# Kernel optimization log

Measured on AMD Instinct MI355X. Metric: run time of the kernel, lower is better.

## Reference

```python
import jax, jax.numpy as jnp
import numpy as np

EPS = 0.05
N = 33554432  # 2**25 annotation steps


def setup_inputs() -> dict:
    key = jax.random.key(0)
    # categories in 1..5 (cat==0 is a no-op skip in the original loop; excluding it
    # keeps the output length static at N+1)
    annotation_series = jax.random.randint(key, (N,), 1, 6, dtype=jnp.int64 if jax.config.jax_enable_x64 else jnp.int32)
    # learned scalar weights of the six Linear(1,1,bias=False) layers, at their init constants
    return {
        "annotation_series": annotation_series,
        "origin_w": jnp.asarray(0.0, jnp.float32),
        "big_decrease_w": jnp.asarray(-0.3, jnp.float32),
        "decrease_w": jnp.asarray(-0.1, jnp.float32),
        "same_w": jnp.asarray(0.0, jnp.float32),
        "increase_w": jnp.asarray(0.1, jnp.float32),
        "big_increase_w": jnp.asarray(0.3, jnp.float32),
    }


def _change_table(origin_w, bd, d, s, inc, bi):
    sg = jax.lax.stop_gradient  # clamp bounds came from .item() in torch -> detached
    c1 = jnp.minimum(bd, sg(jnp.minimum(0.0, d))) - EPS                 # big decrease
    c2 = jnp.clip(d, sg(bd) + EPS, 0.0 - EPS)                           # decrease
    c3 = s                                                              # same
    c4 = jnp.clip(inc, 0.0 + EPS, sg(bi) - EPS)                         # increase
    c5 = jnp.maximum(bi, sg(jnp.maximum(0.0, inc)) + EPS)               # big increase
    zero = jnp.zeros_like(c1)  # cat 0 unused (inputs restricted to 1..5)
    return jnp.stack([zero, c1, c2, c3, c4, c5])  # [6]


def reference(annotation_series, origin_w, big_decrease_w, decrease_w, same_w, increase_w, big_increase_w):
    table = _change_table(origin_w, big_decrease_w, decrease_w, same_w, increase_w, big_increase_w)
    changes = table[annotation_series]                    # [N] gather from 6-entry LUT
    series = origin_w + jnp.cumsum(changes)               # [N] inclusive prefix sum
    return jnp.concatenate([origin_w[None], series])      # [N+1]
```

## Files before the change

kernel.cpp:

```cpp
#include <hip/hip_runtime.h>

#define EPS_C 0.05f
#define BLOCK 256
#define SUBT 2
#define CHUNK (SUBT * 4096)

__device__ __forceinline__ void build_table(const float* bd_p, const float* d_p,
                                            const float* s_p, const float* inc_p,
                                            const float* bi_p, float* cs) {
  if (threadIdx.x == 0) {
    float bd = *bd_p, d = *d_p, s = *s_p, inc = *inc_p, bi = *bi_p;
    cs[0] = 0.0f;
    cs[1] = fminf(bd, fminf(0.0f, d)) - EPS_C;
    cs[2] = fminf(fmaxf(d, bd + EPS_C), -EPS_C);
    cs[3] = s;
    cs[4] = fminf(fmaxf(inc, EPS_C), bi - EPS_C);
    cs[5] = fmaxf(bi, fmaxf(0.0f, inc) + EPS_C);
    cs[6] = 0.0f; cs[7] = 0.0f;
  }
}

__global__ __launch_bounds__(BLOCK) void k_reduce_pack(
    const int* __restrict__ ann, const float* bd, const float* d,
    const float* s, const float* inc, const float* bi,
    uint2* __restrict__ packed, float* __restrict__ sums) {
  __shared__ float cs[8];
  __shared__ float wsum[BLOCK / 64];
  build_table(bd, d, s, inc, bi, cs);
  __syncthreads();

  const int b = blockIdx.x, t = threadIdx.x;
  const int4* in4 = (const int4*)(ann + (size_t)b * CHUNK);

  float sum = 0.0f;
#pragma unroll
  for (int j = 0; j < SUBT; ++j) {
    unsigned int w0 = 0u, w1 = 0u;
#pragma unroll
    for (int i = 0; i < 4; ++i) {
      int4 v = in4[j * 1024 + t * 4 + i];
      sum += cs[v.x] + cs[v.y] + cs[v.z] + cs[v.w];
      unsigned int nib = (unsigned)v.x | ((unsigned)v.y << 4) |
                         ((unsigned)v.z << 8) | ((unsigned)v.w << 12);
      if (i < 2) w0 |= nib << ((i & 1) * 16);
      else       w1 |= nib << ((i & 1) * 16);
    }
    packed[(size_t)b * (SUBT * BLOCK) + j * BLOCK + t] = make_uint2(w0, w1);
  }

#pragma unroll
  for (int off = 32; off >= 1; off >>= 1) sum += __shfl_down(sum, off, 64);
  const int lane = t & 63, wid = t >> 6;
  if (lane == 0) wsum[wid] = sum;
  __syncthreads();
  if (t == 0) sums[b] = wsum[0] + wsum[1] + wsum[2] + wsum[3];
}

__global__ __launch_bounds__(BLOCK) void k_scan_out(
    const uint2* __restrict__ packed, const float* __restrict__ sums,
    const float* __restrict__ origin, const float* bd, const float* d,
    const float* s, const float* inc, const float* bi,
    float* __restrict__ out, int nb) {
  __shared__ float cs[8];
  __shared__ float wsum[BLOCK / 64];
  __shared__ float s_base;
  build_table(bd, d, s, inc, bi, cs);
  __syncthreads();

  const int b = blockIdx.x, t = threadIdx.x;
  const int lane = t & 63, wid = t >> 6;

  uint2 w[SUBT];
#pragma unroll
  for (int j = 0; j < SUBT; ++j)
    w[j] = packed[(size_t)b * (SUBT * BLOCK) + j * BLOCK + t];

  float p = 0.0f;
  for (int i = t; i < b; i += BLOCK) p += sums[i];
#pragma unroll
  for (int off = 32; off >= 1; off >>= 1) p += __shfl_down(p, off, 64);
  if (lane == 0) wsum[wid] = p;
  __syncthreads();
  if (t == 0) s_base = *origin + wsum[0] + wsum[1] + wsum[2] + wsum[3];
  __syncthreads();

  float carry = s_base;
#pragma unroll
  for (int j = 0; j < SUBT; ++j) {
    float vals[16];
#pragma unroll
    for (int k = 0; k < 8; ++k) vals[k] = cs[(w[j].x >> (4 * k)) & 0xF];
#pragma unroll
    for (int k = 0; k < 8; ++k) vals[8 + k] = cs[(w[j].y >> (4 * k)) & 0xF];

    float run = 0.0f;
#pragma unroll
    for (int i = 0; i < 16; ++i) run += vals[i];

    float x = run;
#pragma unroll
    for (int off = 1; off < 64; off <<= 1) {
      float y = __shfl_up(x, off, 64);
      if (lane >= off) x += y;
    }
    __syncthreads();
    if (lane == 63) wsum[wid] = x;
    __syncthreads();
    float wexcl = 0.0f, tot = 0.0f;
#pragma unroll
    for (int i = 0; i < BLOCK / 64; ++i) {
      float wv = wsum[i];
      if (i < wid) wexcl += wv;
      tot += wv;
    }
    const float off0 = carry + wexcl + (x - run);

    float4* out4 = (float4*)(out + (size_t)b * CHUNK + j * 4096);
    float r = off0;
#pragma unroll
    for (int i = 0; i < 4; ++i) {
      float4 o;
      o.x = r; r += vals[i * 4 + 0];
      o.y = r; r += vals[i * 4 + 1];
      o.z = r; r += vals[i * 4 + 2];
      o.w = r; r += vals[i * 4 + 3];
      out4[t * 4 + i] = o;
    }
    carry += tot;

    if (b == nb - 1 && t == BLOCK - 1 && j == SUBT - 1)
      out[(size_t)nb * CHUNK] = r;
  }
}

extern "C" void kernel_launch(void* const* d_in, const int* in_sizes, int n_in,
                              void* d_out, int out_size, void* d_ws, size_t ws_size,
                              hipStream_t stream) {
  const int*   ann    = (const int*)d_in[0];
  const float* origin = (const float*)d_in[1];
  const float* bd     = (const float*)d_in[2];
  const float* dw     = (const float*)d_in[3];
  const float* sw     = (const float*)d_in[4];
  const float* inc    = (const float*)d_in[5];
  const float* bi     = (const float*)d_in[6];
  float* out = (float*)d_out;

  const int N  = in_sizes[0];
  const int nb = N / CHUNK;

  float* sums   = (float*)d_ws;
  uint2* packed = (uint2*)((char*)d_ws + 32768);

  k_reduce_pack<<<nb, BLOCK, 0, stream>>>(ann, bd, dw, sw, inc, bi, packed, sums);
  k_scan_out<<<nb, BLOCK, 0, stream>>>(packed, sums, origin, bd, dw, sw, inc, bi,
                                       out, nb);
}
```

Baseline: 272.2 us.

## Split scan into finer blocks with two-level partial sums and nontemporal loads

The reduce kernel now records a partial sum for each wave and sub-tile as well as each block's total. The scan kernel launches four times as many blocks, each handling 2048 elements with 4 elements per thread, and reads the 4-bit packed data as 16-bit words. Each block's base offset is built from the coarse block totals plus a few fine partials, which gives more parallelism and fewer values live per thread. Input loads also use nontemporal hints. The cost is more blocks, each rescanning a longer coarse prefix with redundant reads, and narrower 16-bit packed loads.

After: 262.0 us. 1.04x faster.

```diff
diff --git a/kernel.cpp b/kernel.cpp
--- a/kernel.cpp
+++ b/kernel.cpp
@@ -4,6 +4,9 @@
 #define BLOCK 256
 #define SUBT 2
 #define CHUNK (SUBT * 4096)
+#define CHUNK2 2048
+
+typedef int i4 __attribute__((ext_vector_type(4)));
 
 __device__ __forceinline__ void build_table(const float* bd_p, const float* d_p,
                                             const float* s_p, const float* inc_p,
@@ -23,22 +26,24 @@
 __global__ __launch_bounds__(BLOCK) void k_reduce_pack(
     const int* __restrict__ ann, const float* bd, const float* d,
     const float* s, const float* inc, const float* bi,
-    uint2* __restrict__ packed, float* __restrict__ sums) {
+    uint2* __restrict__ packed, float* __restrict__ coarse,
+    float* __restrict__ fine) {
   __shared__ float cs[8];
-  __shared__ float wsum[BLOCK / 64];
+  __shared__ float wsum[SUBT * 4];
   build_table(bd, d, s, inc, bi, cs);
   __syncthreads();
 
   const int b = blockIdx.x, t = threadIdx.x;
-  const int4* in4 = (const int4*)(ann + (size_t)b * CHUNK);
+  const int lane = t & 63, wid = t >> 6;
+  const i4* in4 = (const i4*)(ann + (size_t)b * CHUNK);
 
-  float sum = 0.0f;
 #pragma unroll
   for (int j = 0; j < SUBT; ++j) {
     unsigned int w0 = 0u, w1 = 0u;
+    float sum = 0.0f;
 #pragma unroll
     for (int i = 0; i < 4; ++i) {
-      int4 v = in4[j * 1024 + t * 4 + i];
+      i4 v = __builtin_nontemporal_load(&in4[j * 1024 + t * 4 + i]);
       sum += cs[v.x] + cs[v.y] + cs[v.z] + cs[v.w];
       unsigned int nib = (unsigned)v.x | ((unsigned)v.y << 4) |
                          ((unsigned)v.z << 8) | ((unsigned)v.w << 12);
@@ -46,37 +51,44 @@
       else       w1 |= nib << ((i & 1) * 16);
     }
     packed[(size_t)b * (SUBT * BLOCK) + j * BLOCK + t] = make_uint2(w0, w1);
+#pragma unroll
+    for (int off = 32; off >= 1; off >>= 1) sum += __shfl_down(sum, off, 64);
+    if (lane == 0) {
+      fine[b * (SUBT * 4) + j * 4 + wid] = sum;
+      wsum[j * 4 + wid] = sum;
+    }
   }
-
+  __syncthreads();
+  if (t == 0) {
+    float tot = 0.0f;
 #pragma unroll
-  for (int off = 32; off >= 1; off >>= 1) sum += __shfl_down(sum, off, 64);
-  const int lane = t & 63, wid = t >> 6;
-  if (lane == 0) wsum[wid] = sum;
-  __syncthreads();
-  if (t == 0) sums[b] = wsum[0] + wsum[1] + wsum[2] + wsum[3];
+    for (int i = 0; i < SUBT * 4; ++i) tot += wsum[i];
+    coarse[b] = tot;
+  }
 }
 
 __global__ __launch_bounds__(BLOCK) void k_scan_out(
-    const uint2* __restrict__ packed, const float* __restrict__ sums,
-    const float* __restrict__ origin, const float* bd, const float* d,
-    const float* s, const float* inc, const float* bi,
-    float* __restrict__ out, int nb) {
+    const unsigned short* __restrict__ uspack, const float* __restrict__ coarse,
+    const float* __restrict__ fine, const float* __restrict__ origin,
+    const float* bd, const float* d, const float* s, const float* inc,
+    const float* bi, float* __restrict__ out, int nb2, int nbc) {
   __shared__ float cs[8];
   __shared__ float wsum[BLOCK / 64];
   __shared__ float s_base;
   build_table(bd, d, s, inc, bi, cs);
   __syncthreads();
 
-  const int b = blockIdx.x, t = threadIdx.x;
+  const int b2 = blockIdx.x, t = threadIdx.x;
   const int lane = t & 63, wid = t >> 6;
+  const int cb = b2 >> 2;
+  const int fcnt = 2 * (b2 & 3);
 
-  uint2 w[SUBT];
-#pragma unroll
-  for (int j = 0; j < SUBT; ++j)
-    w[j] = packed[(size_t)b * (SUBT * BLOCK) + j * BLOCK + t];
+  unsigned short us0 = uspack[(size_t)b2 * 512 + t];
+  unsigned short us1 = uspack[(size_t)b2 * 512 + 256 + t];
 
   float p = 0.0f;
-  for (int i = t; i < b; i += BLOCK) p += sums[i];
+  for (int i = t; i < cb; i += BLOCK) p += coarse[i];
+  if (t < fcnt) p += fine[cb * 8 + t];
 #pragma unroll
   for (int off = 32; off >= 1; off >>= 1) p += __shfl_down(p, off, 64);
   if (lane == 0) wsum[wid] = p;
@@ -85,17 +97,13 @@
   __syncthreads();
 
   float carry = s_base;
+  unsigned short usv[2] = {us0, us1};
 #pragma unroll
-  for (int j = 0; j < SUBT; ++j) {
-    float vals[16];
-#pragma unroll
-    for (int k = 0; k < 8; ++k) vals[k] = cs[(w[j].x >> (4 * k)) & 0xF];
-#pragma unroll
-    for (int k = 0; k < 8; ++k) vals[8 + k] = cs[(w[j].y >> (4 * k)) & 0xF];
-
-    float run = 0.0f;
-#pragma unroll
-    for (int i = 0; i < 16; ++i) run += vals[i];
+  for (int r = 0; r < 2; ++r) {
+    const unsigned short us = usv[r];
+    float v0 = cs[us & 0xF], v1 = cs[(us >> 4) & 0xF];
+    float v2 = cs[(us >> 8) & 0xF], v3 = cs[(us >> 12) & 0xF];
+    float run = v0 + v1 + v2 + v3;
 
     float x = run;
 #pragma unroll
@@ -115,21 +123,16 @@
     }
     const float off0 = carry + wexcl + (x - run);
 
-    float4* out4 = (float4*)(out + (size_t)b * CHUNK + j * 4096);
-    float r = off0;
-#pragma unroll
-    for (int i = 0; i < 4; ++i) {
-      float4 o;
-      o.x = r; r += vals[i * 4 + 0];
-      o.y = r; r += vals[i * 4 + 1];
-      o.z = r; r += vals[i * 4 + 2];
-      o.w = r; r += vals[i * 4 + 3];
-      out4[t * 4 + i] = o;
-    }
+    float4 o;
+    o.x = off0;
+    o.y = off0 + v0;
+    o.z = off0 + v0 + v1;
+    o.w = off0 + v0 + v1 + v2;
+    ((float4*)(out + (size_t)b2 * CHUNK2 + r * 1024))[t] = o;
     carry += tot;
 
-    if (b == nb - 1 && t == BLOCK - 1 && j == SUBT - 1)
-      out[(size_t)nb * CHUNK] = r;
+    if (b2 == nb2 - 1 && t == BLOCK - 1 && r == 1)
+      out[(size_t)nb2 * CHUNK2] = off0 + run;
   }
 }
 
@@ -145,13 +148,17 @@
   const float* bi     = (const float*)d_in[6];
   float* out = (float*)d_out;
 
-  const int N  = in_sizes[0];
-  const int nb = N / CHUNK;
+  const int N   = in_sizes[0];
+  const int nbc = N / CHUNK;
+  const int nb2 = N / CHUNK2;
 
-  float* sums   = (float*)d_ws;
-  uint2* packed = (uint2*)((char*)d_ws + 32768);
+  float* coarse = (float*)d_ws;
+  float* fine   = (float*)((char*)d_ws + 65536);
+  uint2* packed = (uint2*)((char*)d_ws + 262144);
 
-  k_reduce_pack<<<nb, BLOCK, 0, stream>>>(ann, bd, dw, sw, inc, bi, packed, sums);
-  k_scan_out<<<nb, BLOCK, 0, stream>>>(packed, sums, origin, bd, dw, sw, inc, bi,
-                                       out, nb);
+  k_reduce_pack<<<nbc, BLOCK, 0, stream>>>(ann, bd, dw, sw, inc, bi,
+                                           packed, coarse, fine);
+  k_scan_out<<<nb2, BLOCK, 0, stream>>>((const unsigned short*)packed, coarse,
+                                        fine, origin, bd, dw, sw, inc, bi,
+                                        out, nb2, nbc);
 }
```
